# Optimization experiments

Hardware: AMD Instinct MI355X
Metric: run time of the kernel (lower is better)

The kernel has to match this reference:

```python
import jax, jax.numpy as jnp
import numpy as np

D_MODEL = 1024
N_HEADS = 16
D_HEAD = D_MODEL // N_HEADS


def setup_inputs() -> dict:
    key = jax.random.key(0)
    ks = jax.random.split(key, 5)
    s_in = 1.0 / np.sqrt(D_MODEL)
    x = jax.random.normal(ks[0], (4, 2048, D_MODEL), dtype=jnp.float32)
    W_qkv = jax.random.uniform(ks[1], (D_MODEL, 3 * D_MODEL), jnp.float32, -s_in, s_in)
    b_qkv = jax.random.uniform(ks[2], (3 * D_MODEL,), jnp.float32, -s_in, s_in)
    W_out = jax.random.uniform(ks[3], (D_MODEL, D_MODEL), jnp.float32, -s_in, s_in)
    b_out = jax.random.uniform(ks[4], (D_MODEL,), jnp.float32, -s_in, s_in)
    return {"x": x, "W_qkv": W_qkv, "b_qkv": b_qkv, "W_out": W_out, "b_out": b_out}


def reference(x, W_qkv, b_qkv, W_out, b_out):
    B, T, C = x.shape
    qkv = x @ W_qkv + b_qkv                       # [B,T,3C]
    q, k, v = jnp.split(qkv, 3, axis=-1)
    # [B,T,C] -> [B,H,T,Dh]
    def heads(t):
        return t.reshape(B, T, N_HEADS, D_HEAD).transpose(0, 2, 1, 3)
    q, k, v = heads(q), heads(k), heads(v)
    scale = 1.0 / np.sqrt(D_HEAD).astype(np.float32)
    attn = jnp.einsum('bhqd,bhkd->bhqk', q, k) * scale   # [B,H,T,T]
    causal = jnp.tril(jnp.ones((T, T), dtype=bool))
    attn = jnp.where(causal, attn, -jnp.inf)
    attn_weights = jax.nn.softmax(attn, axis=-1)
    out = jnp.einsum('bhqk,bhkd->bhqd', attn_weights, v)  # [B,H,T,Dh]
    out = out.transpose(0, 2, 1, 3).reshape(B, T, C)
    return out @ W_out + b_out
```

## Files before the change

kernel.cpp:

```cpp
#include <hip/hip_runtime.h>
#include <hip/hip_bf16.h>

#define BATCH   4
#define SEQ     2048
#define DMODEL  1024
#define NHEADS  16
#define DHEAD   64
#define MROWS   (BATCH*SEQ)
#define QKV_N   (3*DMODEL)
#define NEG_BIG (-1.0e30f)
#define WS_NEED ((size_t)MROWS * 2*DMODEL * sizeof(__hip_bfloat16))
#define SCALE_Q 0.18033688011112042f

using bf16 = __hip_bfloat16;
typedef __attribute__((ext_vector_type(8))) short short8;
typedef __attribute__((ext_vector_type(4))) float floatx4;

__device__ __align__(16) unsigned short g_wqT[QKV_N * DMODEL];
__device__ __align__(16) unsigned short g_woT[DMODEL * DMODEL];
__device__ __align__(16) unsigned short g_xb [MROWS * DMODEL];

__device__ __forceinline__ unsigned short f2bf_rne(float f) {
    union { bf16 b; unsigned short u; } t;
    t.b = __float2bfloat16(f);
    return t.u;
}

__device__ __forceinline__ void gload_lds16(const void* g, void* l) {
    __builtin_amdgcn_global_load_lds(
        (const __attribute__((address_space(1))) unsigned*)g,
        (__attribute__((address_space(3))) unsigned*)l, 16, 0, 0);
}

__global__ __launch_bounds__(256) void cast_x(const float* __restrict__ x) {
    const size_t i = ((size_t)blockIdx.x*256 + threadIdx.x)*8;
    const float4 a = *(const float4*)(x + i);
    const float4 b = *(const float4*)(x + i + 4);
    union { uint4 u4; unsigned short us[8]; } o;
    o.us[0]=f2bf_rne(a.x); o.us[1]=f2bf_rne(a.y); o.us[2]=f2bf_rne(a.z); o.us[3]=f2bf_rne(a.w);
    o.us[4]=f2bf_rne(b.x); o.us[5]=f2bf_rne(b.y); o.us[6]=f2bf_rne(b.z); o.us[7]=f2bf_rne(b.w);
    *(uint4*)(g_xb + i) = o.u4;
}

__global__ __launch_bounds__(256) void transcast_w2(
    const float* __restrict__ Wq, const float* __restrict__ Wo)
{
    const int bx = blockIdx.x;
    const float* W;
    unsigned short* dst;
    int N, n0;
    if (bx < 48) { W = Wq; dst = g_wqT; N = QKV_N;  n0 = bx * 64; }
    else         { W = Wo; dst = g_woT; N = DMODEL; n0 = (bx - 48) * 64; }
    const int k0 = blockIdx.y * 64;

    __shared__ unsigned short T[64][72];
    const int tid = threadIdx.x;
    const int r = tid >> 2, c0 = (tid & 3) * 16;

#pragma unroll
    for (int it = 0; it < 4; ++it) {
        const float4 v = *(const float4*)(W + (size_t)(k0 + r)*N + n0 + c0 + it*4);
        T[r][c0 + it*4 + 0] = f2bf_rne(v.x);
        T[r][c0 + it*4 + 1] = f2bf_rne(v.y);
        T[r][c0 + it*4 + 2] = f2bf_rne(v.z);
        T[r][c0 + it*4 + 3] = f2bf_rne(v.w);
    }
    __syncthreads();
    const int nr = tid >> 2, kc0 = (tid & 3) * 16;
#pragma unroll
    for (int it = 0; it < 2; ++it) {
        union { uint4 u4; unsigned short us[8]; } o;
#pragma unroll
        for (int j = 0; j < 8; j++) o.us[j] = T[kc0 + it*8 + j][nr];
        *(uint4*)(dst + (size_t)(n0 + nr)*DMODEL + k0 + kc0 + it*8) = o.u4;
    }
}

template<int QKV_MODE>
__device__ __forceinline__ void gemm_body(
    const void* __restrict__ Av, const float* __restrict__ bias,
    void* __restrict__ C0, void* __restrict__ C1, void* __restrict__ C2)
{
    const unsigned short* A  = QKV_MODE ? g_xb  : (const unsigned short*)Av;
    const unsigned short* BT = QKV_MODE ? g_wqT : g_woT;
    constexpr int NBN = QKV_MODE ? 24 : 8;
    constexpr int NWG = NBN * 32;

    __shared__ __align__(16) char smem[98304];
    char* const sA = smem;
    char* const sB = smem + 65536;

    const int orig = blockIdx.x;
    const int wgid = (orig & 7) * (NWG >> 3) + (orig >> 3);
    const int bm = wgid / NBN, bn = wgid % NBN;

    const int tid  = threadIdx.x;
    const int w    = tid >> 6, lane = tid & 63;
    const int m16  = lane & 15, quad = lane >> 4;
    const int rw   = w >> 1, cw = w & 1;

    const int rL = lane >> 2;
    const int cD = (lane & 3) ^ ((lane >> 3) & 3);
    const unsigned short* gA = A  + (size_t)(bm*256 + rL)*DMODEL + cD*8;
    const unsigned short* gB = BT + (size_t)(bn*128 + rL)*DMODEL + cD*8;

    const int laneRd = m16*64 + (quad ^ ((m16 >> 1) & 3))*16;

    floatx4 acc[2][2][4];
#pragma unroll
    for (int q = 0; q < 2; ++q)
#pragma unroll
        for (int i = 0; i < 2; ++i)
#pragma unroll
            for (int j = 0; j < 4; ++j) {
                acc[q][i][j][0]=0.f; acc[q][i][j][1]=0.f;
                acc[q][i][j][2]=0.f; acc[q][i][j][3]=0.f;
            }

    auto stageA = [&](int buf, int a, int k0) {
        const int rg = 4*a + (w >> 1), kh = w & 1;
        gload_lds16(gA + (size_t)(rg*16)*DMODEL + k0 + kh*32,
                    sA + buf*32768 + (rg*2 + kh)*1024);
    };
    auto stageB = [&](int buf, int b, int k0) {
        const int rg = 4*b + (w >> 1), kh = w & 1;
        gload_lds16(gB + (size_t)(rg*16)*DMODEL + k0 + kh*32,
                    sB + buf*16384 + (rg*2 + kh)*1024);
    };

    stageB(0, 0, 0); stageB(0, 1, 0);
    stageA(0, 0, 0); stageA(0, 1, 0); stageA(0, 2, 0); stageA(0, 3, 0);
    asm volatile("s_waitcnt vmcnt(0)" ::: "memory");
    __builtin_amdgcn_s_barrier();

    const int NT = DMODEL / 64;
    for (int t = 0; t < NT; ++t) {
        const int  buf = t & 1;
        const int  k1  = (t + 1) * 64;
        const bool st  = (t + 1 < NT);
        char* const Ab = sA + buf*32768;
        char* const Bb = sB + buf*16384;

        short8 bf[4][2], af[2][2];
#pragma unroll
        for (int j = 0; j < 4; ++j)
#pragma unroll
            for (int kh = 0; kh < 2; ++kh)
                bf[j][kh] = *(const short8*)(Bb + ((cw*4 + j)*2 + kh)*1024 + laneRd);
#pragma unroll
        for (int i = 0; i < 2; ++i)
#pragma unroll
            for (int kh = 0; kh < 2; ++kh)
                af[i][kh] = *(const short8*)(Ab + ((rw*2 + i)*2 + kh)*1024 + laneRd);

        if (st) { stageB(buf^1, 0, k1); stageB(buf^1, 1, k1);
                  stageA(buf^1, 0, k1); stageA(buf^1, 1, k1); }
        __builtin_amdgcn_s_barrier();

        __builtin_amdgcn_s_setprio(1);
#pragma unroll
        for (int i = 0; i < 2; ++i)
#pragma unroll
            for (int j = 0; j < 4; ++j) {
                acc[0][i][j] = __builtin_amdgcn_mfma_f32_16x16x32_bf16(
                    af[i][0], bf[j][0], acc[0][i][j], 0, 0, 0);
                acc[0][i][j] = __builtin_amdgcn_mfma_f32_16x16x32_bf16(
                    af[i][1], bf[j][1], acc[0][i][j], 0, 0, 0);
            }
        __builtin_amdgcn_s_setprio(0);

        if (st) { asm volatile("s_waitcnt vmcnt(4)" ::: "memory"); }
        else    { asm volatile("s_waitcnt vmcnt(0)" ::: "memory"); }
        __builtin_amdgcn_s_barrier();

#pragma unroll
        for (int i = 0; i < 2; ++i)
#pragma unroll
            for (int kh = 0; kh < 2; ++kh)
                af[i][kh] = *(const short8*)(Ab + ((8 + rw*2 + i)*2 + kh)*1024 + laneRd);

        if (st) { stageA(buf^1, 2, k1); stageA(buf^1, 3, k1); }
        __builtin_amdgcn_s_barrier();

        __builtin_amdgcn_s_setprio(1);
#pragma unroll
        for (int i = 0; i < 2; ++i)
#pragma unroll
            for (int j = 0; j < 4; ++j) {
                acc[1][i][j] = __builtin_amdgcn_mfma_f32_16x16x32_bf16(
                    af[i][0], bf[j][0], acc[1][i][j], 0, 0, 0);
                acc[1][i][j] = __builtin_amdgcn_mfma_f32_16x16x32_bf16(
                    af[i][1], bf[j][1], acc[1][i][j], 0, 0, 0);
            }
        __builtin_amdgcn_s_setprio(0);

        if (st) { asm volatile("s_waitcnt vmcnt(2)" ::: "memory"); }
        else    { asm volatile("s_waitcnt vmcnt(0)" ::: "memory"); }
        __builtin_amdgcn_s_barrier();
    }

    float bv[4];
#pragma unroll
    for (int j = 0; j < 4; ++j)
        bv[j] = bias[bn*128 + cw*64 + j*16 + m16];

    if (QKV_MODE) {
        const int seg = bn >> 3;
        if (seg < 2) {
            bf16* Cout = (bf16*)(seg ? C1 : C0);
            const float sc = seg ? 1.0f : SCALE_Q;
#pragma unroll
            for (int q = 0; q < 2; ++q)
#pragma unroll
                for (int i = 0; i < 2; ++i)
#pragma unroll
                    for (int r = 0; r < 4; ++r) {
                        const int gm = bm*256 + q*128 + rw*32 + i*16 + quad*4 + r;
#pragma unroll
                        for (int j = 0; j < 4; ++j) {
                            const int cc = ((bn & 7)*128 + cw*64 + j*16 + m16);
                            Cout[(size_t)gm*DMODEL + cc] =
                                __float2bfloat16((acc[q][i][j][r] + bv[j]) * sc);
                        }
                    }
        } else {
            bf16* VT = (bf16*)C2;
#pragma unroll
            for (int q = 0; q < 2; ++q)
#pragma unroll
                for (int i = 0; i < 2; ++i) {
                    const int gm0 = bm*256 + q*128 + rw*32 + i*16 + quad*4;
                    const int bb = gm0 >> 11, t0 = gm0 & 2047;
#pragma unroll
                    for (int j = 0; j < 4; ++j) {
                        const int cv = (bn & 7)*128 + cw*64 + j*16 + m16;
                        const int hh = cv >> 6, dd = cv & 63;
                        union { unsigned long long u8; unsigned short us[4]; } o;
#pragma unroll
                        for (int r = 0; r < 4; ++r)
                            o.us[r] = f2bf_rne(acc[q][i][j][r] + bv[j]);
                        *(unsigned long long*)(VT
                            + ((size_t)((bb*NHEADS + hh)*DHEAD + dd))*SEQ + t0) = o.u8;
                    }
                }
        }
    } else {
        float* Cout = (float*)C0;
#pragma unroll
        for (int q = 0; q < 2; ++q)
#pragma unroll
            for (int i = 0; i < 2; ++i)
#pragma unroll
                for (int r = 0; r < 4; ++r) {
                    const int gm = bm*256 + q*128 + rw*32 + i*16 + quad*4 + r;
#pragma unroll
                    for (int j = 0; j < 4; ++j) {
                        const int cc = bn*128 + cw*64 + j*16 + m16;
                        Cout[(size_t)gm*DMODEL + cc] = acc[q][i][j][r] + bv[j];
                    }
                }
    }
}

__global__ __launch_bounds__(512, 2) void qkv_proj(
    const float* __restrict__ bias, bf16* Q, bf16* K, bf16* VT)
{
    gemm_body<1>(nullptr, bias, Q, K, VT);
}
__global__ __launch_bounds__(512, 2) void out_proj(
    const void* __restrict__ Av, const float* __restrict__ bias, float* C)
{
    gemm_body<0>(Av, bias, C, nullptr, nullptr);
}

__global__ __launch_bounds__(256, 3) void attn_mfma6(
    const bf16* __restrict__ Qg, const bf16* __restrict__ Kg,
    const bf16* __restrict__ VTg, bf16* __restrict__ Og)
{
    __shared__ alignas(16) unsigned short Kt[2][64][72];
    __shared__ alignas(16) unsigned short Vt[64][72];
    __shared__ alignas(16) unsigned short Ps[4][32][72];

    const int L  = blockIdx.x;
    const int qt = 15 - (L >> 6);
    const int bh = L & 63;
    const int b  = bh >> 4, h = bh & 15;

    const int tid = threadIdx.x;
    const int w = tid >> 6, lane = tid & 63;
    const int m16 = lane & 15, quad = lane >> 4;
    const int sr = tid >> 2, sc0 = (tid & 3) * 8;
    const size_t bhs = (size_t)(b*NHEADS + h);

    const int nkt = 2*qt + 2;
    const int qrow0 = qt*128 + w*32;

    short8 qf[2][2];
#pragma unroll
    for (int i = 0; i < 2; ++i)
#pragma unroll
        for (int c = 0; c < 2; ++c)
            qf[i][c] = *(const short8*)(Qg + (size_t)(b*SEQ + qrow0 + i*16 + m16)*DMODEL
                                        + h*DHEAD + c*32 + quad*8);

    floatx4 of[2][4];
    float mrow[2], lrow[2];
#pragma unroll
    for (int i = 0; i < 2; ++i) {
        mrow[i] = NEG_BIG; lrow[i] = 0.f;
#pragma unroll
        for (int nt = 0; nt < 4; ++nt) { of[i][nt][0]=0.f; of[i][nt][1]=0.f; of[i][nt][2]=0.f; of[i][nt][3]=0.f; }
    }

    {
        const bf16* kp = Kg  + (size_t)(b*SEQ + sr)*DMODEL + h*DHEAD + sc0;
        const bf16* vp = VTg + (bhs*DHEAD + sr)*SEQ + sc0;
        const uint4 a0 = *(const uint4*)kp, a1 = *(const uint4*)(kp + 32);
        const uint4 b0 = *(const uint4*)vp, b1 = *(const uint4*)(vp + 32);
        *(uint4*)&Kt[0][sr][sc0]      = a0;
        *(uint4*)&Kt[0][sr][sc0 + 32] = a1;
        *(uint4*)&Vt[sr][sc0]         = b0;
        *(uint4*)&Vt[sr][sc0 + 32]    = b1;
        __syncthreads();
    }

    for (int kt = 0; kt < nkt; ++kt) {
        const int buf = kt & 1;
        const int k064 = kt * 64;
        const bool pre = (kt + 1 < nkt);
        uint4 kr0, kr1, vr0, vr1;
        if (pre) {
            const bf16* kp = Kg  + (size_t)(b*SEQ + k064 + 64 + sr)*DMODEL + h*DHEAD + sc0;
            const bf16* vp = VTg + (bhs*DHEAD + sr)*SEQ + k064 + 64 + sc0;
            kr0 = *(const uint4*)kp; kr1 = *(const uint4*)(kp + 32);
            vr0 = *(const uint4*)vp; vr1 = *(const uint4*)(vp + 32);
        }

        floatx4 sf[2][4];
#pragma unroll
        for (int t4 = 0; t4 < 4; ++t4) {
            const short8 kf0 = *(const short8*)&Kt[buf][t4*16 + m16][quad*8];
            const short8 kf1 = *(const short8*)&Kt[buf][t4*16 + m16][32 + quad*8];
#pragma unroll
            for (int i = 0; i < 2; ++i) {
                floatx4 a; a[0]=0.f; a[1]=0.f; a[2]=0.f; a[3]=0.f;
                a = __builtin_amdgcn_mfma_f32_16x16x32_bf16(kf0, qf[i][0], a, 0, 0, 0);
                a = __builtin_amdgcn_mfma_f32_16x16x32_bf16(kf1, qf[i][1], a, 0, 0, 0);
                sf[i][t4] = a;
            }
        }

        const bool need_mask = (k064 + 63 > qrow0);
#pragma unroll
        for (int i = 0; i < 2; ++i) {
            if (need_mask) {
                const int qg = qrow0 + i*16 + m16;
#pragma unroll
                for (int t4 = 0; t4 < 4; ++t4)
#pragma unroll
                    for (int r = 0; r < 4; ++r)
                        if (k064 + t4*16 + quad*4 + r > qg) sf[i][t4][r] = NEG_BIG;
            }
            float mx = sf[i][0][0];
#pragma unroll
            for (int t4 = 0; t4 < 4; ++t4)
#pragma unroll
                for (int r = 0; r < 4; ++r) mx = fmaxf(mx, sf[i][t4][r]);
            mx = fmaxf(mx, __shfl_xor(mx, 16));
            mx = fmaxf(mx, __shfl_xor(mx, 32));

            if (__any(mx > mrow[i] + 8.f)) {
                const float mnew  = fmaxf(mrow[i], mx);
                const float alpha = exp2f(mrow[i] - mnew);
                mrow[i] = mnew;
                lrow[i] *= alpha;
#pragma unroll
                for (int nt = 0; nt < 4; ++nt)
#pragma unroll
                    for (int r = 0; r < 4; ++r) of[i][nt][r] *= alpha;
            }

            float rs = 0.f;
#pragma unroll
            for (int t4 = 0; t4 < 4; ++t4) {
#pragma unroll
                for (int r = 0; r < 4; ++r) {
                    const float pv = exp2f(sf[i][t4][r] - mrow[i]);
                    sf[i][t4][r] = pv;
                    rs += pv;
                }
            }
            rs += __shfl_xor(rs, 16);
            rs += __shfl_xor(rs, 32);
            lrow[i] += rs;

#pragma unroll
            for (int t4 = 0; t4 < 4; ++t4) {
                union { unsigned long long u8; unsigned short us[4]; } o;
#pragma unroll
                for (int r = 0; r < 4; ++r) o.us[r] = f2bf_rne(sf[i][t4][r]);
                *(unsigned long long*)&Ps[w][i*16 + m16][t4*16 + quad*4] = o.u8;
            }
        }

        short8 pf[2][2];
#pragma unroll
        for (int i = 0; i < 2; ++i)
#pragma unroll
            for (int c = 0; c < 2; ++c)
                pf[i][c] = *(const short8*)&Ps[w][i*16 + m16][c*32 + quad*8];
#pragma unroll
        for (int nt = 0; nt < 4; ++nt) {
            const short8 vf0 = *(const short8*)&Vt[nt*16 + m16][quad*8];
            const short8 vf1 = *(const short8*)&Vt[nt*16 + m16][32 + quad*8];
#pragma unroll
            for (int i = 0; i < 2; ++i) {
                of[i][nt] = __builtin_amdgcn_mfma_f32_16x16x32_bf16(vf0, pf[i][0], of[i][nt], 0, 0, 0);
                of[i][nt] = __builtin_amdgcn_mfma_f32_16x16x32_bf16(vf1, pf[i][1], of[i][nt], 0, 0, 0);
            }
        }

        __syncthreads();
        if (pre) {
            *(uint4*)&Kt[buf^1][sr][sc0]      = kr0;
            *(uint4*)&Kt[buf^1][sr][sc0 + 32] = kr1;
            *(uint4*)&Vt[sr][sc0]             = vr0;
            *(uint4*)&Vt[sr][sc0 + 32]        = vr1;
        }
        __syncthreads();
    }

#pragma unroll
    for (int i = 0; i < 2; ++i) {
        const float rl = 1.f / fmaxf(lrow[i], 1e-20f);
        const size_t rowbase = (size_t)(b*SEQ + qrow0 + i*16 + m16)*DMODEL + h*DHEAD;
#pragma unroll
        for (int nt = 0; nt < 4; ++nt) {
            union { unsigned long long u8; unsigned short us[4]; } o;
#pragma unroll
            for (int r = 0; r < 4; ++r) o.us[r] = f2bf_rne(of[i][nt][r] * rl);
            *(unsigned long long*)(Og + rowbase + nt*16 + quad*4) = o.u8;
        }
    }
}

__global__ void diag_fill(float* out, int n, float val) {
    int i = blockIdx.x*blockDim.x + threadIdx.x;
    if (i < n) out[i] = val;
}

extern "C" void kernel_launch(void* const* d_in, const int* in_sizes, int n_in,
                              void* d_out, int out_size, void* d_ws, size_t ws_size,
                              hipStream_t stream) {
    const float* x     = (const float*)d_in[0];
    const float* W_qkv = (const float*)d_in[1];
    const float* b_qkv = (const float*)d_in[2];
    const float* W_out = (const float*)d_in[3];
    const float* b_out = (const float*)d_in[4];

    if (ws_size < WS_NEED) {
        const float val = 100.f + (float)(ws_size >> 20);
        diag_fill<<<(out_size + 255)/256, 256, 0, stream>>>((float*)d_out, out_size, val);
        return;
    }

    bf16* Qb  = (bf16*)d_out;
    bf16* VTb = (bf16*)d_out + (size_t)MROWS*DMODEL;
    bf16* Kb  = (bf16*)d_ws;
    bf16* Ob  = (bf16*)d_ws + (size_t)MROWS*DMODEL;

    cast_x<<<MROWS*DMODEL/2048, 256, 0, stream>>>(x);
    {
        dim3 g(64, DMODEL/64);
        transcast_w2<<<g, 256, 0, stream>>>(W_qkv, W_out);
    }
    qkv_proj<<<768, 512, 0, stream>>>(b_qkv, Qb, Kb, VTb);
    attn_mfma6<<<1024, 256, 0, stream>>>(Qb, Kb, VTb, Ob);
    out_proj<<<256, 512, 0, stream>>>(Ob, b_out, (float*)d_out);
}
```

Before: 269.4 us.

## Split QKV projection into dedicated 256x256-tile kernel with interleaved load/compute pipeline

Replaces the shared templated GEMM body for the QKV projection with its own kernel that uses 256x256 output tiles (128 KB LDS, 384 workgroups) instead of 256x128. The K loop is broken into four phases that interleave global-to-LDS loads for the next stage with MFMA work on the current one, with hand-tuned vmcnt waits. The larger tile raises arithmetic intensity and reuse of A and B, at the cost of more LDS per workgroup (likely one workgroup per CU instead of two) and fewer workgroups, which risks occupancy and tail effects.

```diff
diff --git a/kernel.cpp b/kernel.cpp
--- a/kernel.cpp
+++ b/kernel.cpp
@@ -76,14 +76,188 @@
     }
 }
 
-template<int QKV_MODE>
-__device__ __forceinline__ void gemm_body(
-    const void* __restrict__ Av, const float* __restrict__ bias,
-    void* __restrict__ C0, void* __restrict__ C1, void* __restrict__ C2)
+__global__ __launch_bounds__(512, 2) void qkv_proj(
+    const float* __restrict__ bias, bf16* __restrict__ Qo,
+    bf16* __restrict__ Ko, bf16* __restrict__ VT)
 {
-    const unsigned short* A  = QKV_MODE ? g_xb  : (const unsigned short*)Av;
-    const unsigned short* BT = QKV_MODE ? g_wqT : g_woT;
-    constexpr int NBN = QKV_MODE ? 24 : 8;
+    const unsigned short* A  = g_xb;
+    const unsigned short* BT = g_wqT;
+    constexpr int NBN = 12;
+    constexpr int NWG = 32 * NBN;
+
+    __shared__ __align__(16) char smem[131072];
+    char* const sA = smem;
+    char* const sB = smem + 65536;
+
+    const int orig = blockIdx.x;
+    const int wgid = (orig & 7) * (NWG >> 3) + (orig >> 3);
+    const int bm = wgid / NBN, bn = wgid % NBN;
+
+    const int tid  = threadIdx.x;
+    const int w    = tid >> 6, lane = tid & 63;
+    const int m16  = lane & 15, quad = lane >> 4;
+    const int rw   = w >> 2, cw = w & 3;
+
+    const int rL = lane >> 2;
+    const int cD = (lane & 3) ^ ((lane >> 3) & 3);
+    const unsigned short* gA = A  + (size_t)(bm*256 + rL)*DMODEL + cD*8;
+    const unsigned short* gB = BT + (size_t)(bn*256 + rL)*DMODEL + cD*8;
+
+    const int laneRd = m16*64 + (quad ^ ((m16 >> 1) & 3))*16;
+
+    floatx4 acc[8][4];
+#pragma unroll
+    for (int i = 0; i < 8; ++i)
+#pragma unroll
+        for (int j = 0; j < 4; ++j) {
+            acc[i][j][0]=0.f; acc[i][j][1]=0.f; acc[i][j][2]=0.f; acc[i][j][3]=0.f;
+        }
+
+    auto stA = [&](int buf, int rg, int kh, int k0) {
+        gload_lds16(gA + (size_t)(rg*16)*DMODEL + k0 + kh*32,
+                    sA + buf*32768 + (rg*2 + kh)*1024);
+    };
+    auto stB = [&](int buf, int rg, int kh, int k0) {
+        gload_lds16(gB + (size_t)(rg*16)*DMODEL + k0 + kh*32,
+                    sB + buf*32768 + (rg*2 + kh)*1024);
+    };
+
+    stB(0, 2*w, 0, 0);   stB(0, 2*w+1, 0, 0);
+    stA(0, w,   0, 0);   stA(0, w,   1, 0);
+    stA(0, 8+w, 0, 0);   stA(0, 8+w, 1, 0);
+    stB(0, 2*w, 1, 0);   stB(0, 2*w+1, 1, 0);
+    asm volatile("s_waitcnt vmcnt(0)" ::: "memory");
+    __builtin_amdgcn_s_barrier();
+
+    const int NT = DMODEL / 64;
+    for (int t = 0; t < NT; ++t) {
+        const int  buf = t & 1;
+        const int  k1  = (t + 1) * 64;
+        const bool st  = (t + 1 < NT);
+        char* const Ab = sA + buf*32768;
+        char* const Bb = sB + buf*32768;
+
+        short8 bf[4], af[4];
+
+#pragma unroll
+        for (int j = 0; j < 4; ++j)
+            bf[j] = *(const short8*)(Bb + ((cw*4 + j)*2 + 0)*1024 + laneRd);
+#pragma unroll
+        for (int i = 0; i < 4; ++i)
+            af[i] = *(const short8*)(Ab + ((rw*8 + i)*2 + 0)*1024 + laneRd);
+        if (st) { stB(buf^1, 2*w, 0, k1); stB(buf^1, 2*w+1, 0, k1); }
+        __builtin_amdgcn_s_barrier();
+        __builtin_amdgcn_s_setprio(1);
+#pragma unroll
+        for (int i = 0; i < 4; ++i)
+#pragma unroll
+            for (int j = 0; j < 4; ++j)
+                acc[i][j] = __builtin_amdgcn_mfma_f32_16x16x32_bf16(af[i], bf[j], acc[i][j], 0, 0, 0);
+        __builtin_amdgcn_s_setprio(0);
+        if (st) { asm volatile("s_waitcnt vmcnt(4)" ::: "memory"); }
+        else    { asm volatile("s_waitcnt vmcnt(2)" ::: "memory"); }
+        __builtin_amdgcn_s_barrier();
+
+#pragma unroll
+        for (int i = 0; i < 4; ++i)
+            af[i] = *(const short8*)(Ab + ((rw*8 + 4 + i)*2 + 0)*1024 + laneRd);
+        if (st) { stA(buf^1, w, 0, k1); stA(buf^1, w, 1, k1); }
+        __builtin_amdgcn_s_barrier();
+        __builtin_amdgcn_s_setprio(1);
+#pragma unroll
+        for (int i = 0; i < 4; ++i)
+#pragma unroll
+            for (int j = 0; j < 4; ++j)
+                acc[4+i][j] = __builtin_amdgcn_mfma_f32_16x16x32_bf16(af[i], bf[j], acc[4+i][j], 0, 0, 0);
+        __builtin_amdgcn_s_setprio(0);
+        if (st) { asm volatile("s_waitcnt vmcnt(4)" ::: "memory"); }
+        else    { asm volatile("s_waitcnt vmcnt(0)" ::: "memory"); }
+        __builtin_amdgcn_s_barrier();
+
+#pragma unroll
+        for (int j = 0; j < 4; ++j)
+            bf[j] = *(const short8*)(Bb + ((cw*4 + j)*2 + 1)*1024 + laneRd);
+#pragma unroll
+        for (int i = 0; i < 4; ++i)
+            af[i] = *(const short8*)(Ab + ((rw*8 + i)*2 + 1)*1024 + laneRd);
+        if (st) { stA(buf^1, 8+w, 0, k1); stA(buf^1, 8+w, 1, k1); }
+        __builtin_amdgcn_s_barrier();
+        __builtin_amdgcn_s_setprio(1);
+#pragma unroll
+        for (int i = 0; i < 4; ++i)
+#pragma unroll
+            for (int j = 0; j < 4; ++j)
+                acc[i][j] = __builtin_amdgcn_mfma_f32_16x16x32_bf16(af[i], bf[j], acc[i][j], 0, 0, 0);
+        __builtin_amdgcn_s_setprio(0);
+        if (st) { asm volatile("s_waitcnt vmcnt(6)" ::: "memory"); }
+        else    { asm volatile("s_waitcnt vmcnt(0)" ::: "memory"); }
+        __builtin_amdgcn_s_barrier();
+
+#pragma unroll
+        for (int i = 0; i < 4; ++i)
+            af[i] = *(const short8*)(Ab + ((rw*8 + 4 + i)*2 + 1)*1024 + laneRd);
+        if (st) { stB(buf^1, 2*w, 1, k1); stB(buf^1, 2*w+1, 1, k1); }
+        __builtin_amdgcn_s_barrier();
+        __builtin_amdgcn_s_setprio(1);
+#pragma unroll
+        for (int i = 0; i < 4; ++i)
+#pragma unroll
+            for (int j = 0; j < 4; ++j)
+                acc[4+i][j] = __builtin_amdgcn_mfma_f32_16x16x32_bf16(af[i], bf[j], acc[4+i][j], 0, 0, 0);
+        __builtin_amdgcn_s_setprio(0);
+        if (st) {
+            asm volatile("s_waitcnt vmcnt(4)" ::: "memory");
+            __builtin_amdgcn_s_barrier();
+        }
+    }
+
+    float bv[4];
+#pragma unroll
+    for (int j = 0; j < 4; ++j)
+        bv[j] = bias[bn*256 + cw*64 + j*16 + m16];
+
+    const int seg = bn >> 2;
+    if (seg < 2) {
+        bf16* Cout = seg ? Ko : Qo;
+        const float sc = seg ? 1.0f : SCALE_Q;
+#pragma unroll
+        for (int mf = 0; mf < 8; ++mf)
+#pragma unroll
+            for (int r = 0; r < 4; ++r) {
+                const int gm = bm*256 + rw*128 + mf*16 + quad*4 + r;
+#pragma unroll
+                for (int j = 0; j < 4; ++j) {
+                    const int cc = (bn*256 + cw*64 + j*16 + m16) & 1023;
+                    Cout[(size_t)gm*DMODEL + cc] =
+                        __float2bfloat16((acc[mf][j][r] + bv[j]) * sc);
+                }
+            }
+    } else {
+#pragma unroll
+        for (int mf = 0; mf < 8; ++mf) {
+            const int gm0 = bm*256 + rw*128 + mf*16 + quad*4;
+            const int bb = gm0 >> 11, t0 = gm0 & 2047;
+#pragma unroll
+            for (int j = 0; j < 4; ++j) {
+                const int cv = ((bn & 3)*256 + cw*64 + j*16 + m16);
+                const int hh = cv >> 6, dd = cv & 63;
+                union { unsigned long long u8; unsigned short us[4]; } o;
+#pragma unroll
+                for (int r = 0; r < 4; ++r)
+                    o.us[r] = f2bf_rne(acc[mf][j][r] + bv[j]);
+                *(unsigned long long*)(VT
+                    + ((size_t)((bb*NHEADS + hh)*DHEAD + dd))*SEQ + t0) = o.u8;
+            }
+        }
+    }
+}
+
+__global__ __launch_bounds__(512, 2) void out_proj(
+    const void* __restrict__ Av, const float* __restrict__ bias, float* C)
+{
+    const unsigned short* A  = (const unsigned short*)Av;
+    const unsigned short* BT = g_woT;
+    constexpr int NBN = 8;
     constexpr int NWG = NBN * 32;
 
     __shared__ __align__(16) char smem[98304];
@@ -204,73 +378,19 @@
     for (int j = 0; j < 4; ++j)
         bv[j] = bias[bn*128 + cw*64 + j*16 + m16];
 
-    if (QKV_MODE) {
-        const int seg = bn >> 3;
-        if (seg < 2) {
-            bf16* Cout = (bf16*)(seg ? C1 : C0);
-            const float sc = seg ? 1.0f : SCALE_Q;
-#pragma unroll
-            for (int q = 0; q < 2; ++q)
-#pragma unroll
-                for (int i = 0; i < 2; ++i)
-#pragma unroll
-                    for (int r = 0; r < 4; ++r) {
-                        const int gm = bm*256 + q*128 + rw*32 + i*16 + quad*4 + r;
-#pragma unroll
-                        for (int j = 0; j < 4; ++j) {
-                            const int cc = ((bn & 7)*128 + cw*64 + j*16 + m16);
-                            Cout[(size_t)gm*DMODEL + cc] =
-                                __float2bfloat16((acc[q][i][j][r] + bv[j]) * sc);
-                        }
-                    }
-        } else {
-            bf16* VT = (bf16*)C2;
-#pragma unroll
-            for (int q = 0; q < 2; ++q)
-#pragma unroll
-                for (int i = 0; i < 2; ++i) {
-                    const int gm0 = bm*256 + q*128 + rw*32 + i*16 + quad*4;
-                    const int bb = gm0 >> 11, t0 = gm0 & 2047;
-#pragma unroll
-                    for (int j = 0; j < 4; ++j) {
-                        const int cv = (bn & 7)*128 + cw*64 + j*16 + m16;
-                        const int hh = cv >> 6, dd = cv & 63;
-                        union { unsigned long long u8; unsigned short us[4]; } o;
-#pragma unroll
-                        for (int r = 0; r < 4; ++r)
-                            o.us[r] = f2bf_rne(acc[q][i][j][r] + bv[j]);
-                        *(unsigned long long*)(VT
-                            + ((size_t)((bb*NHEADS + hh)*DHEAD + dd))*SEQ + t0) = o.u8;
-                    }
+#pragma unroll
+    for (int q = 0; q < 2; ++q)
+#pragma unroll
+        for (int i = 0; i < 2; ++i)
+#pragma unroll
+            for (int r = 0; r < 4; ++r) {
+                const int gm = bm*256 + q*128 + rw*32 + i*16 + quad*4 + r;
+#pragma unroll
+                for (int j = 0; j < 4; ++j) {
+                    const int cc = bn*128 + cw*64 + j*16 + m16;
+                    C[(size_t)gm*DMODEL + cc] = acc[q][i][j][r] + bv[j];
                 }
-        }
-    } else {
-        float* Cout = (float*)C0;
-#pragma unroll
-        for (int q = 0; q < 2; ++q)
-#pragma unroll
-            for (int i = 0; i < 2; ++i)
-#pragma unroll
-                for (int r = 0; r < 4; ++r) {
-                    const int gm = bm*256 + q*128 + rw*32 + i*16 + quad*4 + r;
-#pragma unroll
-                    for (int j = 0; j < 4; ++j) {
-                        const int cc = bn*128 + cw*64 + j*16 + m16;
-                        Cout[(size_t)gm*DMODEL + cc] = acc[q][i][j][r] + bv[j];
-                    }
-                }
-    }
-}
-
-__global__ __launch_bounds__(512, 2) void qkv_proj(
-    const float* __restrict__ bias, bf16* Q, bf16* K, bf16* VT)
-{
-    gemm_body<1>(nullptr, bias, Q, K, VT);
-}
-__global__ __launch_bounds__(512, 2) void out_proj(
-    const void* __restrict__ Av, const float* __restrict__ bias, float* C)
-{
-    gemm_body<0>(Av, bias, C, nullptr, nullptr);
+            }
 }
 
 __global__ __launch_bounds__(256, 3) void attn_mfma6(
@@ -474,7 +594,7 @@
         dim3 g(64, DMODEL/64);
         transcast_w2<<<g, 256, 0, stream>>>(W_qkv, W_out);
     }
-    qkv_proj<<<768, 512, 0, stream>>>(b_qkv, Qb, Kb, VTb);
+    qkv_proj<<<384, 512, 0, stream>>>(b_qkv, Qb, Kb, VTb);
     attn_mfma6<<<1024, 256, 0, stream>>>(Qb, Kb, VTb, Ob);
     out_proj<<<256, 512, 0, stream>>>(Ob, b_out, (float*)d_out);
 }
```

Result: no change. 264.8 us (-1.7%).
